# Optimization experiments

Hardware: AMD Instinct MI355X
Metric: run time of the kernel (lower is better)

Reference implementation:

```python
import jax, jax.numpy as jnp
import numpy as np
from jax import lax

EPS = 1e-5
NBIT = 127.0  # 8-bit symmetric: 2^(8-1)-1

def ste_round(x):
    return x + lax.stop_gradient(jnp.round(x) - x)

def quant_act(x, rng_max):
    # symmetric fake-quant of activations with learned per-cluster range
    s = rng_max / NBIT
    xq = jnp.clip(ste_round(x / s), -NBIT, NBIT) * s
    return xq, s

def fold_bn(w, gamma, beta, mean, var):
    std = jnp.sqrt(var + EPS)
    scale = gamma / std
    w_f = w * scale[:, None, None, None]
    b_f = beta - mean * scale
    return w_f, b_f

def quant_weight(w):
    # per-output-channel symmetric quant
    s = jnp.max(jnp.abs(w), axis=(1, 2, 3), keepdims=True) / NBIT
    wq = jnp.clip(ste_round(w / s), -NBIT, NBIT) * s
    return wq, s.reshape(-1)

def conv(x, w, stride=1, groups=1, pad=0):
    return lax.conv_general_dilated(
        x, w, window_strides=(stride, stride),
        padding=((pad, pad), (pad, pad)),
        dimension_numbers=('NCHW', 'OIHW', 'NCHW'),
        feature_group_count=groups)

def setup_inputs() -> dict:
    key = jax.random.key(0)
    ks = jax.random.split(key, 24)
    B, Cin, H, W = 64, 96, 28, 28
    Cmid, Cout, NC = 576, 96, 4
    d = {}
    d['x'] = jax.random.normal(ks[0], (B, Cin, H, W), dtype=jnp.float32)
    # conv1: 1x1 expansion
    d['w1'] = jax.random.normal(ks[1], (Cmid, Cin, 1, 1), jnp.float32) * 0.1
    d['g1'] = jax.random.uniform(ks[2], (Cmid,), minval=0.5, maxval=1.5)
    d['b1'] = jax.random.normal(ks[3], (Cmid,)) * 0.1
    d['m1'] = jax.random.normal(ks[4], (Cmid,)) * 0.1
    d['v1'] = jax.random.uniform(ks[5], (Cmid,), minval=0.5, maxval=1.5)
    # conv2: 3x3 depthwise
    d['w2'] = jax.random.normal(ks[6], (Cmid, 1, 3, 3), jnp.float32) * 0.1
    d['g2'] = jax.random.uniform(ks[7], (Cmid,), minval=0.5, maxval=1.5)
    d['b2'] = jax.random.normal(ks[8], (Cmid,)) * 0.1
    d['m2'] = jax.random.normal(ks[9], (Cmid,)) * 0.1
    d['v2'] = jax.random.uniform(ks[10], (Cmid,), minval=0.5, maxval=1.5)
    # conv3: 1x1 projection
    d['w3'] = jax.random.normal(ks[11], (Cout, Cmid, 1, 1), jnp.float32) * 0.1
    d['g3'] = jax.random.uniform(ks[12], (Cout,), minval=0.5, maxval=1.5)
    d['b3'] = jax.random.normal(ks[13], (Cout,)) * 0.1
    d['m3'] = jax.random.normal(ks[14], (Cout,)) * 0.1
    d['v3'] = jax.random.uniform(ks[15], (Cout,), minval=0.5, maxval=1.5)
    # per-cluster learned activation ranges for the 4 QuantAct modules
    d['r0'] = jax.random.uniform(ks[16], (NC,), minval=2.0, maxval=8.0)
    d['r1'] = jax.random.uniform(ks[17], (NC,), minval=2.0, maxval=8.0)
    d['r2'] = jax.random.uniform(ks[18], (NC,), minval=2.0, maxval=8.0)
    d['r3'] = jax.random.uniform(ks[19], (NC,), minval=2.0, maxval=8.0)
    d['cluster'] = 2
    return d

def reference(x, w1, g1, b1, m1, v1, w2, g2, b2, m2, v2,
              w3, g3, b3, m3, v3, r0, r1, r2, r3, cluster):
    identity = x  # residual path (in==out, stride==1)
    # QuantAct -> conv1 (BN-folded, per-channel quant) -> ReLU6
    xq, s0 = quant_act(x, r0[cluster])
    w1f, bf1 = fold_bn(w1, g1, b1, m1, v1)
    w1q, ws1 = quant_weight(w1f)
    y = conv(xq, w1q) + bf1[None, :, None, None]
    y = jnp.clip(y, 0.0, 6.0)
    # QuantAct1 -> depthwise conv2 -> ReLU6
    yq, s1 = quant_act(y, r1[cluster])
    w2f, bf2 = fold_bn(w2, g2, b2, m2, v2)
    w2q, ws2 = quant_weight(w2f)
    y = conv(yq, w2q, stride=1, groups=w2.shape[0], pad=1) + bf2[None, :, None, None]
    y = jnp.clip(y, 0.0, 6.0)
    # QuantAct2 -> conv3 projection
    yq, s2 = quant_act(y, r2[cluster])
    w3f, bf3 = fold_bn(w3, g3, b3, m3, v3)
    w3q, ws3 = quant_weight(w3f)
    y = conv(yq, w3q) + bf3[None, :, None, None]
    # residual add, then int32 requant
    y = y + identity
    out, s3 = quant_act(y, r3[cluster])
    return out, s3
```

## Files before the change

kernel.cpp:

```cpp
#include <hip/hip_runtime.h>
#include <cstdint>
#include <cstddef>

typedef int   v4i __attribute__((ext_vector_type(4)));
typedef float v4f __attribute__((ext_vector_type(4)));
typedef unsigned int u32;

constexpr int B_   = 64;
constexpr int CIN  = 96;
constexpr int P_   = 784;
constexpr int CMID = 576;
constexpr int COUT = 96;
constexpr int NOUT = B_ * COUT * P_;
constexpr float NBITF = 127.0f;
constexpr float EPSF  = 1e-5f;
constexpr float MAGICF = 12582912.0f;
constexpr int   BIASI  = 0x4B400000;

constexpr int XB4 = 13 * 8 * 64;
constexpr int Y1S = 29;

__device__ __forceinline__ int dot3(u32 a, u32 w, int acc) {
#if __has_builtin(__builtin_amdgcn_sdot4)
    return __builtin_amdgcn_sdot4((int)a, (int)w, acc, false);
#else
    return acc + (int)(signed char)(a)        * (int)(signed char)(w)
               + (int)(signed char)(a >> 8)   * (int)(signed char)(w >> 8)
               + (int)(signed char)(a >> 16)  * (int)(signed char)(w >> 16);
#endif
}

__device__ __forceinline__ void tr4(u32 S0, u32 S1, u32 S2, u32 S3, u32 O[4]) {
    u32 u01 = __builtin_amdgcn_perm(S1, S0, 0x05010400u);
    u32 u23 = __builtin_amdgcn_perm(S3, S2, 0x05010400u);
    u32 v01 = __builtin_amdgcn_perm(S1, S0, 0x07030602u);
    u32 v23 = __builtin_amdgcn_perm(S3, S2, 0x07030602u);
    O[0] = __builtin_amdgcn_perm(u23, u01, 0x05040100u);
    O[1] = __builtin_amdgcn_perm(u23, u01, 0x07060302u);
    O[2] = __builtin_amdgcn_perm(v23, v01, 0x05040100u);
    O[3] = __builtin_amdgcn_perm(v23, v01, 0x07060302u);
}

__device__ __forceinline__ u32 pack4(u32 t0, u32 t1, u32 t2, u32 t3) {
    u32 p01 = __builtin_amdgcn_perm(t1, t0, 0x05010400u);
    u32 p23 = __builtin_amdgcn_perm(t3, t2, 0x05010400u);
    return __builtin_amdgcn_perm(p23, p01, 0x05040100u);
}

__global__ __launch_bounds__(256)
void prep_all(const float* __restrict__ x,
              const float* __restrict__ w1, const float* __restrict__ g1,
              const float* __restrict__ b1, const float* __restrict__ m1,
              const float* __restrict__ v1,
              const float* __restrict__ w2, const float* __restrict__ g2,
              const float* __restrict__ b2, const float* __restrict__ m2,
              const float* __restrict__ v2,
              const float* __restrict__ w3, const float* __restrict__ g3,
              const float* __restrict__ b3, const float* __restrict__ m3,
              const float* __restrict__ v3,
              const float* __restrict__ r0, const float* __restrict__ r1,
              const float* __restrict__ r2, const int* __restrict__ cluster,
              u32* __restrict__ x8t2,
              int8_t* __restrict__ w1qp, float2* __restrict__ e1,
              v4i* __restrict__ w2pk,    float2* __restrict__ e2,
              int8_t* __restrict__ w3qp, float2* __restrict__ e3)
{
    __shared__ u32 T[112 * 37];
    int tid = threadIdx.x;
    int c = cluster[0];

    if (blockIdx.x < 448) {
        int pt0 = blockIdx.x % 7, b = blockIdx.x / 7;
        float inv_s0 = NBITF / r0[c];

        for (int i = tid; i < 112 * 8; i += 256) {
            int row = i >> 3, cc = 24 + (i & 7);
            T[row * 37 + cc] = 0u;
        }
        for (int u = tid; u < 24 * 28; u += 256) {
            int pq = u % 28, icq = u / 28;
            int pxb = pt0 * 112 + pq * 4;
            int q[4][4];
            #pragma unroll
            for (int j = 0; j < 4; j++) {
                v4f xv = *(const v4f*)(x + ((size_t)b * CIN + icq * 4 + j) * P_ + pxb);
                #pragma unroll
                for (int i = 0; i < 4; i++)
                    q[j][i] = (int)fminf(fmaxf(rintf(xv[i] * inv_s0), -127.f), 127.f);
            }
            #pragma unroll
            for (int i = 0; i < 4; i++) {
                u32 t0 = __builtin_amdgcn_perm((u32)q[1][i], (u32)q[0][i], 0x00000400u);
                u32 t1 = __builtin_amdgcn_perm((u32)q[3][i], (u32)q[2][i], 0x00000400u);
                T[(pq * 4 + i) * 37 + icq] = __builtin_amdgcn_perm(t1, t0, 0x05040100u);
            }
        }
        __syncthreads();
        u32* gb = x8t2 + (size_t)b * XB4 * 4;
        for (int i = tid; i < 32 * 112; i += 256) {
            int icq = i / 112, pxo = i - icq * 112;
            int px = pt0 * 112 + pxo;
            gb[(((px >> 6) * 8 + (icq >> 2)) * 64 + (px & 63)) * 4 + (icq & 3)] =
                T[pxo * 37 + icq];
        }
        return;
    }

    int lane = tid & 63, wv = tid >> 6;
    int blk = (blockIdx.x - 448) * 4 + wv;

    const float *w, *g, *bb, *mm, *vv;
    int oc, K, which;
    if (blk < CMID)            { which = 0; w = w1; g = g1; bb = b1; mm = m1; vv = v1; oc = blk;            K = CIN;  }
    else if (blk < 2 * CMID)   { which = 1; w = w2; g = g2; bb = b2; mm = m2; vv = v2; oc = blk - CMID;     K = 9;    }
    else                       { which = 2; w = w3; g = g3; bb = b3; mm = m3; vv = v3; oc = blk - 2 * CMID; K = CMID; }

    float scale = g[oc] / sqrtf(vv[oc] + EPSF);

    float mx = 0.f;
    for (int k = lane; k < K; k += 64)
        mx = fmaxf(mx, fabsf(w[oc * K + k] * scale));
    #pragma unroll
    for (int off = 1; off < 64; off <<= 1)
        mx = fmaxf(mx, __shfl_xor(mx, off));

    float s = mx / NBITF;

    int myq = 0;
    for (int k = lane; k < K; k += 64) {
        float wf = w[oc * K + k] * scale;
        float q  = fminf(fmaxf(rintf(wf / s), -127.f), 127.f);
        if (which == 0)      w1qp[oc * 144 + k] = (int8_t)q;
        else if (which == 1) myq = (int)q;
        else                 w3qp[oc * 592 + k] = (int8_t)q;
    }
    if (which == 0 && lane < 12)
        ((u32*)(w1qp + oc * 144))[24 + lane] = 0u;
    if (which == 1) {
        u32 qq[9];
        #pragma unroll
        for (int t = 0; t < 9; t++) qq[t] = (u32)__shfl(myq, t, 64) & 0xffu;
        if (lane == 0) {
            v4i pk;
            pk[0] = (int)(qq[0] | (qq[1] << 8) | (qq[2] << 16));
            pk[1] = (int)(qq[3] | (qq[4] << 8) | (qq[5] << 16));
            pk[2] = (int)(qq[6] | (qq[7] << 8) | (qq[8] << 16));
            pk[3] = 0;
            w2pk[oc] = pk;
        }
    }
    if (lane == 0) {
        float bf = bb[oc] - mm[oc] * scale;
        float s0 = r0[c] / NBITF, s1 = r1[c] / NBITF, s2 = r2[c] / NBITF;
        if (which == 0) {
            float inv_s1 = NBITF / r1[c];
            e1[oc] = make_float2(s0 * s * inv_s1, bf * inv_s1);
        } else if (which == 1) {
            float inv_s2 = NBITF / r2[c];
            e2[oc] = make_float2(s1 * s * inv_s2, bf * inv_s2);
        } else {
            e3[oc] = make_float2(s2 * s, bf);
        }
    }
}

__global__ __launch_bounds__(256, 3)
void conv123d(const v4i* __restrict__ x8t2, const v4i* __restrict__ w1q4,
              const float2* __restrict__ e1,
              const v4i* __restrict__ w2pk, const float2* __restrict__ e2,
              const int8_t* __restrict__ w3qp, const float2* __restrict__ e3,
              const float* __restrict__ x,
              const float* __restrict__ r1, const float* __restrict__ r2,
              const float* __restrict__ r3, const int* __restrict__ cluster,
              float* __restrict__ out)
{
    __shared__ v4i xw[7 * 8 * 16];
    __shared__ u32 y1s[4][48 * Y1S];
    __shared__ v4i y2c[12 * 56];

    int tid = threadIdx.x, b = blockIdx.y, rt = blockIdx.x;
    int R0 = 2 * rt;
    int W0 = (R0 - 1) * 28;
    int lane = tid & 63, wv = tid >> 6;
    int n = lane & 15, q4 = lane >> 4;

    int   c      = cluster[0];
    int   u1i    = (int)fminf(rintf(6.f * NBITF / r1[c]), 127.f);
    int   u2i    = (int)fminf(rintf(6.f * NBITF / r2[c]), 127.f);
    float s3     = r3[c] / NBITF;
    float inv_s3 = NBITF / r3[c];

    const v4i* xb = x8t2 + (size_t)b * XB4;
    for (int i = tid; i < 7 * 8 * 16; i += 256) {
        int jm = i >> 7, g = (i >> 4) & 7, nn = i & 15;
        int px = min(max(W0 + 16 * jm + nn, 0), P_ - 1);
        xw[i] = xb[(px >> 6) * 512 + g * 64 + (px & 63)];
    }

    u32* myY1 = y1s[wv];

    int pxl = wv * 16 + n;
    int pxc = min(pxl, 55);
    const v4i* w34 = (const v4i*)w3qp;
    v4i acc3[6];
    #pragma unroll
    for (int i = 0; i < 6; i++) acc3[i] = (v4i){0, 0, 0, 0};

    __syncthreads();

    for (int ph = 0; ph < 3; ph++) {
        int oc0 = ph * 192 + wv * 48;

        v4i    bw[3][2];
        float2 ee[3];
        #pragma unroll
        for (int jn = 0; jn < 3; jn++) {
            int oc = oc0 + 16 * jn + n;
            bw[jn][0] = w1q4[oc * 9 + q4];
            bw[jn][1] = w1q4[oc * 9 + 4 + q4];
            ee[jn] = e1[oc];
        }
        #pragma unroll
        for (int jm = 0; jm < 7; jm++) {
            v4i af0 = xw[(jm * 8 + q4) * 16 + n];
            v4i af1 = xw[(jm * 8 + 4 + q4) * 16 + n];
            int dw = 4 * jm + q4;
            bool valid = (unsigned)(W0 + 4 * dw) < (unsigned)P_;

            #pragma unroll
            for (int jn = 0; jn < 3; jn++) {
                v4i acc = (v4i){0, 0, 0, 0};
                acc = __builtin_amdgcn_mfma_i32_16x16x64_i8(af0, bw[jn][0], acc, 0, 0, 0);
                acc = __builtin_amdgcn_mfma_i32_16x16x64_i8(af1, bw[jn][1], acc, 0, 0, 0);
                u32 t[4];
                #pragma unroll
                for (int r = 0; r < 4; r++) {
                    float f = fmaf((float)acc[r], ee[jn].x, ee[jn].y) + MAGICF;
                    t[r] = (u32)min(max(__float_as_int(f), BIASI), BIASI + u1i);
                }
                u32 pk = pack4(t[0], t[1], t[2], t[3]);
                myY1[(16 * jn + n) * Y1S + dw] = valid ? pk : 0u;
            }
        }

        #pragma unroll
        for (int p = 0; p < 3; p++) {
            int id   = p * 64 + lane;
            int chl  = id >> 2;
            int orow = (id >> 1) & 1;
            int half = id & 1;
            int ch   = oc0 + chl;
            int rb   = chl * Y1S + orow * 7;
            int wbse = chl * Y1S + orow * 21 + half * 4;

            v4i wpk = w2pk[ch];
            u32 pk0 = (u32)wpk[0], pk1 = (u32)wpk[1], pk2 = (u32)wpk[2];
            float2 e = e2[ch];

            u32 P[3], S[3][4], Q[3];
            #pragma unroll
            for (int i = 0; i < 3; i++) {
                int rbi = rb + 7 * i;
                u32 s0 = myY1[rbi + half * 4 + 0];
                u32 s1 = myY1[rbi + half * 4 + 1];
                u32 s2 = myY1[rbi + half * 4 + 2];
                u32 t3 = myY1[rbi + 3];
                u32 t4 = myY1[rbi + 4];
                S[i][0] = s0; S[i][1] = s1; S[i][2] = s2;
                P[i]    = half ? t3 : 0u;
                S[i][3] = half ? 0u : t3;
                Q[i]    = half ? 0u : t4;
            }

            #pragma unroll
            for (int xq = 0; xq < 4; xq++) {
                u32 M0 = (xq == 0) ? P[0] : S[0][xq - 1];
                u32 M1 = (xq == 0) ? P[1] : S[1][xq - 1];
                u32 M2 = (xq == 0) ? P[2] : S[2][xq - 1];
                u32 D0 = S[0][xq], D1 = S[1][xq], D2 = S[2][xq];
                u32 N0 = (xq == 3) ? Q[0] : S[0][xq + 1];
                u32 N1 = (xq == 3) ? Q[1] : S[1][xq + 1];
                u32 N2 = (xq == 3) ? Q[2] : S[2][xq + 1];

                int a0, a1, a2, a3;
                a0 = dot3(__builtin_amdgcn_alignbyte(D0, M0, 3), pk0, 0);
                a0 = dot3(__builtin_amdgcn_alignbyte(D1, M1, 3), pk1, a0);
                a0 = dot3(__builtin_amdgcn_alignbyte(D2, M2, 3), pk2, a0);
                a1 = dot3(D0, pk0, 0);
                a1 = dot3(D1, pk1, a1);
                a1 = dot3(D2, pk2, a1);
                a2 = dot3(__builtin_amdgcn_alignbyte(N0, D0, 1), pk0, 0);
                a2 = dot3(__builtin_amdgcn_alignbyte(N1, D1, 1), pk1, a2);
                a2 = dot3(__builtin_amdgcn_alignbyte(N2, D2, 1), pk2, a2);
                a3 = dot3(__builtin_amdgcn_alignbyte(N0, D0, 2), pk0, 0);
                a3 = dot3(__builtin_amdgcn_alignbyte(N1, D1, 2), pk1, a3);
                a3 = dot3(__builtin_amdgcn_alignbyte(N2, D2, 2), pk2, a3);

                int aa[4] = {a0, a1, a2, a3};
                u32 tq[4];
                #pragma unroll
                for (int i = 0; i < 4; i++) {
                    float f = fmaf((float)aa[i], e.x, e.y) + MAGICF;
                    tq[i] = (u32)min(max(__float_as_int(f), BIASI), BIASI + u2i);
                }
                if (!half || xq < 3)
                    myY1[wbse + xq] = pack4(tq[0], tq[1], tq[2], tq[3]);
            }
        }

        if (lane < 42) {
            int kgl = lane / 14, d = lane - kgl * 14;
            int off = d + ((d >= 7) ? 14 : 0);
            u32 O[4][4];
            #pragma unroll
            for (int j = 0; j < 4; j++) {
                int ch0 = 16 * kgl + 4 * j;
                tr4(myY1[(ch0 + 0) * Y1S + off], myY1[(ch0 + 1) * Y1S + off],
                    myY1[(ch0 + 2) * Y1S + off], myY1[(ch0 + 3) * Y1S + off], O[j]);
            }
            int kgG = wv * 3 + kgl;
            #pragma unroll
            for (int i = 0; i < 4; i++)
                y2c[kgG * 56 + 4 * d + i] =
                    (v4i){(int)O[0][i], (int)O[1][i], (int)O[2][i], (int)O[3][i]};
        }

        __syncthreads();

        #pragma unroll
        for (int ks = 0; ks < 3; ks++) {
            v4i bfr = y2c[(4 * ks + q4) * 56 + pxc];
            #pragma unroll
            for (int i = 0; i < 6; i++) {
                v4i afr = w34[(i * 16 + n) * 37 + ph * 12 + 4 * ks + q4];
                acc3[i] = __builtin_amdgcn_mfma_i32_16x16x64_i8(afr, bfr, acc3[i], 0, 0, 0);
            }
        }

        if (ph < 2) __syncthreads();
    }

    if (pxl < 56) {
        int px = R0 * 28 + pxl;
        #pragma unroll
        for (int i = 0; i < 6; i++) {
            #pragma unroll
            for (int r = 0; r < 4; r++) {
                int    oc = i * 16 + q4 * 4 + r;
                float2 e  = e3[oc];
                size_t gi = (size_t)(b * COUT + oc) * P_ + px;
                float v  = fmaf((float)acc3[i][r], e.x, e.y) + x[gi];
                float f  = fmaf(v, inv_s3, MAGICF);
                int lvl  = min(max(__float_as_int(f) - BIASI, -127), 127);
                out[gi]  = (float)lvl * s3;
            }
        }
    }
    if (rt == 0 && b == 0 && tid == 0)
        out[NOUT] = s3;
}

extern "C" void kernel_launch(void* const* d_in, const int* in_sizes, int n_in,
                              void* d_out, int out_size, void* d_ws, size_t ws_size,
                              hipStream_t stream)
{
    const float* x  = (const float*)d_in[0];
    const float* w1 = (const float*)d_in[1];
    const float* g1 = (const float*)d_in[2];
    const float* b1 = (const float*)d_in[3];
    const float* m1 = (const float*)d_in[4];
    const float* v1 = (const float*)d_in[5];
    const float* w2 = (const float*)d_in[6];
    const float* g2 = (const float*)d_in[7];
    const float* b2 = (const float*)d_in[8];
    const float* m2 = (const float*)d_in[9];
    const float* v2 = (const float*)d_in[10];
    const float* w3 = (const float*)d_in[11];
    const float* g3 = (const float*)d_in[12];
    const float* b3 = (const float*)d_in[13];
    const float* m3 = (const float*)d_in[14];
    const float* v3 = (const float*)d_in[15];
    const float* r0 = (const float*)d_in[16];
    const float* r1 = (const float*)d_in[17];
    const float* r2 = (const float*)d_in[18];
    const float* r3 = (const float*)d_in[19];
    const int*   cl = (const int*)d_in[20];

    float* out = (float*)d_out;

    char*  ws  = (char*)d_ws;
    size_t off = 0;
    auto carve = [&](size_t bytes) {
        size_t cur = off;
        off = (off + bytes + 255) & ~(size_t)255;
        return (void*)(ws + cur);
    };
    int8_t* w1qp = (int8_t*)carve((size_t)CMID * 144);
    float2* e1   = (float2*)carve((size_t)CMID * 8);
    v4i*    w2pk = (v4i*)carve((size_t)CMID * 16);
    float2* e2   = (float2*)carve((size_t)CMID * 8);
    int8_t* w3qp = (int8_t*)carve((size_t)COUT * 592);
    float2* e3   = (float2*)carve((size_t)COUT * 8);
    u32*    x8t2 = (u32*)carve((size_t)B_ * XB4 * 16);
    (void)ws_size; (void)in_sizes; (void)n_in; (void)out_size;

    prep_all<<<dim3(760), dim3(256), 0, stream>>>(
        x, w1, g1, b1, m1, v1, w2, g2, b2, m2, v2, w3, g3, b3, m3, v3,
        r0, r1, r2, cl, x8t2,
        w1qp, e1, w2pk, e2, w3qp, e3);

    conv123d<<<dim3(14, B_), dim3(256), 0, stream>>>(
        (const v4i*)x8t2, (const v4i*)w1qp, e1, w2pk, e2, w3qp, e3,
        x, r1, r2, r3, cl, out);
}
```

Baseline: 161.5 us.

## Fuse input activation quantization into main conv kernel, drop x8t2 staging buffer

Moves the int8 quantization and channel packing of the input x from the prep kernel into the fused conv kernel's shared-memory tile load. This removes the global write and read of the packed x8t2 buffer and shrinks the prep grid to weight-only work. In exchange, each conv block reads fp32 x directly with strided per-channel loads and recomputes quantization for halo rows that neighbouring tiles also load, so it adds redundant reads and compute.

```diff
diff --git a/kernel.cpp b/kernel.cpp
--- a/kernel.cpp
+++ b/kernel.cpp
@@ -17,7 +17,6 @@
 constexpr float MAGICF = 12582912.0f;
 constexpr int   BIASI  = 0x4B400000;
 
-constexpr int XB4 = 13 * 8 * 64;
 constexpr int Y1S = 29;
 
 __device__ __forceinline__ int dot3(u32 a, u32 w, int acc) {
@@ -48,66 +47,25 @@
 }
 
 __global__ __launch_bounds__(256)
-void prep_all(const float* __restrict__ x,
-              const float* __restrict__ w1, const float* __restrict__ g1,
-              const float* __restrict__ b1, const float* __restrict__ m1,
-              const float* __restrict__ v1,
-              const float* __restrict__ w2, const float* __restrict__ g2,
-              const float* __restrict__ b2, const float* __restrict__ m2,
-              const float* __restrict__ v2,
-              const float* __restrict__ w3, const float* __restrict__ g3,
-              const float* __restrict__ b3, const float* __restrict__ m3,
-              const float* __restrict__ v3,
-              const float* __restrict__ r0, const float* __restrict__ r1,
-              const float* __restrict__ r2, const int* __restrict__ cluster,
-              u32* __restrict__ x8t2,
-              int8_t* __restrict__ w1qp, float2* __restrict__ e1,
-              v4i* __restrict__ w2pk,    float2* __restrict__ e2,
-              int8_t* __restrict__ w3qp, float2* __restrict__ e3)
+void prep_w(const float* __restrict__ w1, const float* __restrict__ g1,
+            const float* __restrict__ b1, const float* __restrict__ m1,
+            const float* __restrict__ v1,
+            const float* __restrict__ w2, const float* __restrict__ g2,
+            const float* __restrict__ b2, const float* __restrict__ m2,
+            const float* __restrict__ v2,
+            const float* __restrict__ w3, const float* __restrict__ g3,
+            const float* __restrict__ b3, const float* __restrict__ m3,
+            const float* __restrict__ v3,
+            const float* __restrict__ r0, const float* __restrict__ r1,
+            const float* __restrict__ r2, const int* __restrict__ cluster,
+            int8_t* __restrict__ w1qp, float2* __restrict__ e1,
+            v4i* __restrict__ w2pk,    float2* __restrict__ e2,
+            int8_t* __restrict__ w3qp, float2* __restrict__ e3)
 {
-    __shared__ u32 T[112 * 37];
     int tid = threadIdx.x;
     int c = cluster[0];
-
-    if (blockIdx.x < 448) {
-        int pt0 = blockIdx.x % 7, b = blockIdx.x / 7;
-        float inv_s0 = NBITF / r0[c];
-
-        for (int i = tid; i < 112 * 8; i += 256) {
-            int row = i >> 3, cc = 24 + (i & 7);
-            T[row * 37 + cc] = 0u;
-        }
-        for (int u = tid; u < 24 * 28; u += 256) {
-            int pq = u % 28, icq = u / 28;
-            int pxb = pt0 * 112 + pq * 4;
-            int q[4][4];
-            #pragma unroll
-            for (int j = 0; j < 4; j++) {
-                v4f xv = *(const v4f*)(x + ((size_t)b * CIN + icq * 4 + j) * P_ + pxb);
-                #pragma unroll
-                for (int i = 0; i < 4; i++)
-                    q[j][i] = (int)fminf(fmaxf(rintf(xv[i] * inv_s0), -127.f), 127.f);
-            }
-            #pragma unroll
-            for (int i = 0; i < 4; i++) {
-                u32 t0 = __builtin_amdgcn_perm((u32)q[1][i], (u32)q[0][i], 0x00000400u);
-                u32 t1 = __builtin_amdgcn_perm((u32)q[3][i], (u32)q[2][i], 0x00000400u);
-                T[(pq * 4 + i) * 37 + icq] = __builtin_amdgcn_perm(t1, t0, 0x05040100u);
-            }
-        }
-        __syncthreads();
-        u32* gb = x8t2 + (size_t)b * XB4 * 4;
-        for (int i = tid; i < 32 * 112; i += 256) {
-            int icq = i / 112, pxo = i - icq * 112;
-            int px = pt0 * 112 + pxo;
-            gb[(((px >> 6) * 8 + (icq >> 2)) * 64 + (px & 63)) * 4 + (icq & 3)] =
-                T[pxo * 37 + icq];
-        }
-        return;
-    }
-
     int lane = tid & 63, wv = tid >> 6;
-    int blk = (blockIdx.x - 448) * 4 + wv;
+    int blk = blockIdx.x * 4 + wv;
 
     const float *w, *g, *bb, *mm, *vv;
     int oc, K, which;
@@ -165,11 +123,12 @@
 }
 
 __global__ __launch_bounds__(256, 3)
-void conv123d(const v4i* __restrict__ x8t2, const v4i* __restrict__ w1q4,
+void conv123d(const v4i* __restrict__ w1q4,
               const float2* __restrict__ e1,
               const v4i* __restrict__ w2pk, const float2* __restrict__ e2,
               const int8_t* __restrict__ w3qp, const float2* __restrict__ e3,
               const float* __restrict__ x,
+              const float* __restrict__ r0,
               const float* __restrict__ r1, const float* __restrict__ r2,
               const float* __restrict__ r3, const int* __restrict__ cluster,
               float* __restrict__ out)
@@ -185,16 +144,33 @@
     int n = lane & 15, q4 = lane >> 4;
 
     int   c      = cluster[0];
+    float inv_s0 = NBITF / r0[c];
     int   u1i    = (int)fminf(rintf(6.f * NBITF / r1[c]), 127.f);
     int   u2i    = (int)fminf(rintf(6.f * NBITF / r2[c]), 127.f);
     float s3     = r3[c] / NBITF;
     float inv_s3 = NBITF / r3[c];
 
-    const v4i* xb = x8t2 + (size_t)b * XB4;
-    for (int i = tid; i < 7 * 8 * 16; i += 256) {
-        int jm = i >> 7, g = (i >> 4) & 7, nn = i & 15;
+    for (int i = tid; i < 2688; i += 256) {
+        int nn = i & 15;
+        int q  = (i >> 4) & 3;
+        int gj = i >> 6;
+        int g  = gj % 6, jm = gj / 6;
         int px = min(max(W0 + 16 * jm + nn, 0), P_ - 1);
-        xw[i] = xb[(px >> 6) * 512 + g * 64 + (px & 63)];
+        const float* xp = x + ((size_t)b * CIN + 16 * g + 4 * q) * P_ + px;
+        int qv[4];
+        #pragma unroll
+        for (int j = 0; j < 4; j++) {
+            float xf = xp[j * P_];
+            qv[j] = (int)fminf(fmaxf(rintf(xf * inv_s0), -127.f), 127.f);
+        }
+        u32 t0 = __builtin_amdgcn_perm((u32)qv[1], (u32)qv[0], 0x00000400u);
+        u32 t1 = __builtin_amdgcn_perm((u32)qv[3], (u32)qv[2], 0x00000400u);
+        ((u32*)xw)[((jm * 8 + g) * 16 + nn) * 4 + q] =
+            __builtin_amdgcn_perm(t1, t0, 0x05040100u);
+    }
+    for (int i = tid; i < 7 * 2 * 16; i += 256) {
+        int nn = i & 15, gg = (i >> 4) & 1, jm = i >> 5;
+        xw[(jm * 8 + 6 + gg) * 16 + nn] = (v4i){0, 0, 0, 0};
     }
 
     u32* myY1 = y1s[wv];
@@ -401,15 +377,14 @@
     float2* e2   = (float2*)carve((size_t)CMID * 8);
     int8_t* w3qp = (int8_t*)carve((size_t)COUT * 592);
     float2* e3   = (float2*)carve((size_t)COUT * 8);
-    u32*    x8t2 = (u32*)carve((size_t)B_ * XB4 * 16);
     (void)ws_size; (void)in_sizes; (void)n_in; (void)out_size;
 
-    prep_all<<<dim3(760), dim3(256), 0, stream>>>(
-        x, w1, g1, b1, m1, v1, w2, g2, b2, m2, v2, w3, g3, b3, m3, v3,
-        r0, r1, r2, cl, x8t2,
+    prep_w<<<dim3(312), dim3(256), 0, stream>>>(
+        w1, g1, b1, m1, v1, w2, g2, b2, m2, v2, w3, g3, b3, m3, v3,
+        r0, r1, r2, cl,
         w1qp, e1, w2pk, e2, w3qp, e3);
 
     conv123d<<<dim3(14, B_), dim3(256), 0, stream>>>(
-        (const v4i*)x8t2, (const v4i*)w1qp, e1, w2pk, e2, w3qp, e3,
-        x, r1, r2, r3, cl, out);
-}
+        (const v4i*)w1qp, e1, w2pk, e2, w3qp, e3,
+        x, r0, r1, r2, r3, cl, out);
+}
```

Result: no change. 163.3 us (+1.1%).
